# Kernel tuning notes

Measured on AMD Instinct MI355X. Metric: run time of the kernel, lower is better.

## Reference

```python
import jax, jax.numpy as jnp
import numpy as np

N = 50000  # num nodes
E = 800000  # num edges
D_IN = 128
D_OUT = 128
K = 2


def mean_propagate(x, src, dst):
    # scatter-mean over incoming edges: out[d] = mean_{(s,d) in edges} x[s]
    sums = jax.ops.segment_sum(x[src], dst, num_segments=N)  # [N, D]
    deg = jax.ops.segment_sum(jnp.ones((src.shape[0],), x.dtype), dst, num_segments=N)
    return sums / jnp.maximum(deg, 1.0)[:, None]


def setup_inputs() -> dict:
    key = jax.random.key(0)
    k1, k2, k3, k4 = jax.random.split(key, 4)
    x = jax.random.normal(k1, (N, D_IN), dtype=jnp.float32)
    edge_index = jax.random.randint(k2, (2, E), 0, N, dtype=jnp.int64)
    fan_in = D_IN * (K + 1)
    bound = 1.0 / np.sqrt(fan_in)
    W = jax.random.uniform(k3, (D_OUT, fan_in), dtype=jnp.float32, minval=-bound, maxval=bound)
    b = jax.random.uniform(k4, (D_OUT,), dtype=jnp.float32, minval=-bound, maxval=bound)
    return {"x": x, "edge_index": edge_index, "W": W, "b": b}


def reference(x, edge_index, W, b):
    src, dst = edge_index[0], edge_index[1]
    features = [x]
    propagated = x
    for _ in range(K):
        propagated = mean_propagate(propagated, src, dst)
        features.append(propagated)
    h = jnp.concatenate(features, axis=-1)  # [N, D_IN*(K+1)]
    return h @ W.T + b  # [N, D_OUT]
```

## Files before the change

### kernel.cpp

```cpp
#include <hip/hip_runtime.h>
#include <cstddef>


#define DFEAT 128
#define SUBSHIFT 8
#define MAXSUB 256
#define EPB 2048
#define CAP 16384

typedef __attribute__((ext_vector_type(8))) short short8v;
typedef __attribute__((ext_vector_type(4))) float f32x4;

__device__ inline unsigned short f2bf(float f) {
    unsigned int u;
    __builtin_memcpy(&u, &f, 4);
    unsigned int r = u + 0x7FFFu + ((u >> 16) & 1u);
    return (unsigned short)(r >> 16);
}
__device__ inline float bf2f(unsigned short h) {
    unsigned int u = ((unsigned int)h) << 16;
    float f;
    __builtin_memcpy(&f, &u, 4);
    return f;
}

__global__ void zero_kernel(int* __restrict__ p, int n) {
    int i = blockIdx.x * blockDim.x + threadIdx.x;
    if (i < n) p[i] = 0;
}

__global__ void conv_bf16_kernel(const float* __restrict__ in,
                                 unsigned short* __restrict__ outb, int total4) {
    int i = blockIdx.x * blockDim.x + threadIdx.x;
    if (i >= total4) return;
    const float4 v = reinterpret_cast<const float4*>(in)[i];
    unsigned int w0 = (unsigned int)f2bf(v.x) | ((unsigned int)f2bf(v.y) << 16);
    unsigned int w1 = (unsigned int)f2bf(v.z) | ((unsigned int)f2bf(v.w) << 16);
    reinterpret_cast<uint2*>(outb)[i] = make_uint2(w0, w1);
}

__global__ void pack_w_kernel(const float* __restrict__ W,
                              unsigned short* __restrict__ Wpk) {
    const int idx = blockIdx.x * blockDim.x + threadIdx.x;
    if (idx >= 6144) return;
    const int lane = idx & 63;
    const int nt = (idx >> 6) & 7;
    const int ks = idx >> 9;
    const int col = nt * 16 + (lane & 15);
    const int k = ks * 32 + (lane >> 4) * 8;
    const float* wp = W + (size_t)col * 384 + k;
    unsigned int w[4];
#pragma unroll
    for (int j = 0; j < 4; ++j) {
        w[j] = (unsigned int)f2bf(wp[2 * j]) |
               ((unsigned int)f2bf(wp[2 * j + 1]) << 16);
    }
    *reinterpret_cast<uint4*>(Wpk + (size_t)idx * 8) = make_uint4(w[0], w[1], w[2], w[3]);
}

__global__ __launch_bounds__(256) void partitionA_kernel(
    const int* __restrict__ src, const int* __restrict__ dst,
    int* __restrict__ subFill, int* __restrict__ subReal,
    uint2* __restrict__ staging, int E, int nsub) {
    __shared__ int cnt[MAXSUB];
    __shared__ int base[MAXSUB];
    const int t = threadIdx.x;
    for (int i = t; i < nsub; i += 256) cnt[i] = 0;
    __syncthreads();
    const int e0 = blockIdx.x * EPB;
    int d[8], s[8], b[8], rk[8];
#pragma unroll
    for (int j = 0; j < 8; ++j) {
        const int e = e0 + j * 256 + t;
        if (e < E) {
            d[j] = __builtin_nontemporal_load(dst + e);
            s[j] = __builtin_nontemporal_load(src + e);
            b[j] = d[j] >> SUBSHIFT;
            rk[j] = atomicAdd(&cnt[b[j]], 1);
        } else {
            d[j] = -1; s[j] = 0; b[j] = 0; rk[j] = 0;
        }
    }
    __syncthreads();
    for (int i = t; i < nsub; i += 256) {
        const int c = cnt[i];
        if (c > 0) {
            const int padded = (c + 15) & ~15;
            int bse = atomicAdd(&subFill[i], padded);
            if (bse + padded > CAP) bse = CAP - padded;
            base[i] = bse;
            atomicAdd(&subReal[i], c);
        }
    }
    __syncthreads();
#pragma unroll
    for (int j = 0; j < 8; ++j)
        if (d[j] >= 0)
            staging[(size_t)b[j] * CAP + base[b[j]] + rk[j]] =
                make_uint2((unsigned)d[j], (unsigned)s[j]);
    for (int i = t; i < nsub; i += 256) {
        const int c = cnt[i];
        if (c > 0) {
            const int padded = (c + 15) & ~15;
            for (int k = c; k < padded; ++k)
                staging[(size_t)i * CAP + base[i] + k] = make_uint2(0xFFFFFFFFu, 0u);
        }
    }
}

__global__ __launch_bounds__(256) void scanSub_kernel(const int* __restrict__ subReal,
                                                      int* __restrict__ subBase, int nsub) {
    __shared__ int s[256];
    const int t = threadIdx.x;
    const int v = (t < nsub) ? subReal[t] : 0;
    s[t] = v;
    __syncthreads();
#pragma unroll
    for (int off = 1; off < 256; off <<= 1) {
        int x = (t >= off) ? s[t - off] : 0;
        __syncthreads();
        s[t] += x;
        __syncthreads();
    }
    if (t < nsub) subBase[t] = s[t] - v;
}

__global__ __launch_bounds__(256) void partitionB_kernel(
    const uint2* __restrict__ staging, const int* __restrict__ subFill,
    const int* __restrict__ subBase, int* __restrict__ rowptr,
    float* __restrict__ inv, int* __restrict__ col, int N, int E) {
    __shared__ int cnt[1 << SUBSHIFT];
    __shared__ int loc[1 << SUBSHIFT];
    __shared__ int cur[1 << SUBSHIFT];
    const int b = blockIdx.x;
    const int n0 = b << SUBSHIFT;
    const int t = threadIdx.x;
    cnt[t] = 0;
    __syncthreads();
    const int fill = min(subFill[b], CAP);
    const uint2* seg = staging + (size_t)b * CAP;
    for (int i = t; i < fill; i += 256) {
        const unsigned dd = seg[i].x;
        if (dd != 0xFFFFFFFFu) atomicAdd(&cnt[dd - (unsigned)n0], 1);
    }
    __syncthreads();
    const int v = cnt[t];
    loc[t] = v;
    __syncthreads();
#pragma unroll
    for (int off = 1; off < 256; off <<= 1) {
        int x = (t >= off) ? loc[t - off] : 0;
        __syncthreads();
        loc[t] += x;
        __syncthreads();
    }
    const int gpos = subBase[b] + loc[t] - v;
    const int n = n0 + t;
    if (n < N) {
        rowptr[n] = gpos;
        inv[n] = 1.0f / (float)max(v, 1);
    }
    cur[t] = gpos;
    __syncthreads();
    for (int i = t; i < fill; i += 256) {
        const uint2 pr = seg[i];
        if (pr.x != 0xFFFFFFFFu) {
            const int pos = atomicAdd(&cur[(int)pr.x - n0], 1);
            col[pos] = (int)pr.y;
        }
    }
    if (b == 0 && t == 0) rowptr[N] = E;
}

__global__ __launch_bounds__(256) void gather_bf16_kernel(
    const unsigned short* __restrict__ feat, const int* __restrict__ rowptr,
    const int* __restrict__ col, const float* __restrict__ inv,
    unsigned short* __restrict__ outb, int N) {
    const int n = blockIdx.x * 16 + (threadIdx.x >> 4);
    const int lane = threadIdx.x & 15;
    if (n >= N) return;
    const int beg = rowptr[n];
    const int end = rowptr[n + 1];
    float acc[8];
#pragma unroll
    for (int j = 0; j < 8; ++j) acc[j] = 0.0f;
    int e = beg;
    for (; e + 1 < end; e += 2) {
        const int s0 = col[e];
        const int s1 = col[e + 1];
        const short8v v0 = *reinterpret_cast<const short8v*>(
            feat + (size_t)s0 * DFEAT + lane * 8);
        const short8v v1 = *reinterpret_cast<const short8v*>(
            feat + (size_t)s1 * DFEAT + lane * 8);
#pragma unroll
        for (int j = 0; j < 8; ++j)
            acc[j] += bf2f((unsigned short)v0[j]) + bf2f((unsigned short)v1[j]);
    }
    if (e < end) {
        const int s0 = col[e];
        const short8v v0 = *reinterpret_cast<const short8v*>(
            feat + (size_t)s0 * DFEAT + lane * 8);
#pragma unroll
        for (int j = 0; j < 8; ++j) acc[j] += bf2f((unsigned short)v0[j]);
    }
    const float sc = inv[n];
    unsigned int w[4];
#pragma unroll
    for (int j = 0; j < 4; ++j) {
        w[j] = (unsigned int)f2bf(acc[2 * j] * sc) |
               ((unsigned int)f2bf(acc[2 * j + 1] * sc) << 16);
    }
    *reinterpret_cast<uint4*>(outb + (size_t)n * DFEAT + lane * 8) =
        make_uint4(w[0], w[1], w[2], w[3]);
}

__global__ __launch_bounds__(256) void gemm_mfma_kernel(
    const unsigned short* __restrict__ xb, const unsigned short* __restrict__ m1b,
    const unsigned short* __restrict__ m2b, const unsigned short* __restrict__ Wpk,
    const float* __restrict__ bias, float* __restrict__ out, int N) {
    const int t = threadIdx.x;
    const int w = t >> 6;
    const int l = t & 63;
    const int lr = l & 15;
    const int kg = l >> 4;
    const int rowBase = blockIdx.x * 64 + w * 16;
    int arow = rowBase + lr;
    if (arow >= N) arow = N - 1;

    const short8v* Wv = reinterpret_cast<const short8v*>(Wpk);

    f32x4 acc[8];
#pragma unroll
    for (int nt = 0; nt < 8; ++nt) acc[nt] = (f32x4){0.f, 0.f, 0.f, 0.f};

#pragma unroll
    for (int ks = 0; ks < 12; ++ks) {
        const unsigned short* feat = (ks < 4) ? xb : (ks < 8 ? m1b : m2b);
        const int k0 = (ks & 3) * 32;
        const short8v a = *reinterpret_cast<const short8v*>(
            feat + (size_t)arow * DFEAT + k0 + kg * 8);
        short8v bfrag[8];
#pragma unroll
        for (int nt = 0; nt < 8; ++nt)
            bfrag[nt] = Wv[(ks * 8 + nt) * 64 + l];
#pragma unroll
        for (int nt = 0; nt < 8; ++nt)
            acc[nt] = __builtin_amdgcn_mfma_f32_16x16x32_bf16(a, bfrag[nt], acc[nt], 0, 0, 0);
    }

#pragma unroll
    for (int nt = 0; nt < 8; ++nt) {
        const int c = nt * 16 + lr;
        const float bv = bias[c];
#pragma unroll
        for (int r = 0; r < 4; ++r) {
            const int node = rowBase + kg * 4 + r;
            if (node < N) out[(size_t)node * DFEAT + c] = acc[nt][r] + bv;
        }
    }
}

extern "C" void kernel_launch(void* const* d_in, const int* in_sizes, int n_in,
                              void* d_out, int out_size, void* d_ws, size_t ws_size,
                              hipStream_t stream) {
    (void)n_in; (void)out_size; (void)ws_size;
    const float* x  = (const float*)d_in[0];
    const int*   ei = (const int*)d_in[1];
    const float* W  = (const float*)d_in[2];
    const float* b  = (const float*)d_in[3];
    float* out = (float*)d_out;

    const int N = in_sizes[0] / DFEAT;
    const int E = in_sizes[1] / 2;
    const int* src = ei;
    const int* dst = ei + E;
    const int nsub = (N + (1 << SUBSHIFT) - 1) >> SUBSHIFT;

    auto up = [](size_t v) { return (v + 255) & ~(size_t)255; };
    char* p = (char*)d_ws;
    int*   subFill   = (int*)p;            p += up((size_t)MAXSUB * 4 * 2);
    int*   subReal   = subFill + MAXSUB;
    int*   subBase   = (int*)p;            p += up((size_t)MAXSUB * 4);
    int*   rowptr    = (int*)p;            p += up(((size_t)N + 1) * 4);
    uint2* staging   = (uint2*)p;          p += up((size_t)MAXSUB * CAP * 8);
    int*   col       = (int*)p;            p += up((size_t)E * 4);
    float* inv       = (float*)p;          p += up((size_t)N * 4);
    unsigned short* xb  = (unsigned short*)p;  p += up((size_t)N * DFEAT * 2);
    unsigned short* m1b = (unsigned short*)p;  p += up((size_t)N * DFEAT * 2);
    unsigned short* m2b = (unsigned short*)p;  p += up((size_t)N * DFEAT * 2);
    unsigned short* Wpk = (unsigned short*)p;  p += up((size_t)6144 * 8 * 2);

    zero_kernel<<<1, 2 * MAXSUB, 0, stream>>>(subFill, 2 * MAXSUB);

    partitionA_kernel<<<(E + EPB - 1) / EPB, 256, 0, stream>>>(src, dst, subFill, subReal,
                                                               staging, E, nsub);
    scanSub_kernel<<<1, 256, 0, stream>>>(subReal, subBase, nsub);
    partitionB_kernel<<<nsub, 256, 0, stream>>>(staging, subFill, subBase,
                                                rowptr, inv, col, N, E);

    const int x4 = N * DFEAT / 4;
    conv_bf16_kernel<<<(x4 + 255) / 256, 256, 0, stream>>>(x, xb, x4);
    pack_w_kernel<<<(6144 + 255) / 256, 256, 0, stream>>>(W, Wpk);

    const int gatherBlocks = (N + 15) / 16;
    gather_bf16_kernel<<<gatherBlocks, 256, 0, stream>>>(xb,  rowptr, col, inv, m1b, N);
    gather_bf16_kernel<<<gatherBlocks, 256, 0, stream>>>(m1b, rowptr, col, inv, m2b, N);

    gemm_mfma_kernel<<<(N + 63) / 64, 256, 0, stream>>>(xb, m1b, m2b, Wpk, b, out, N);
}
```

Baseline: 142.0 us.

## Split bf16 features into 32-column planes and gather each plane separately

The bf16 feature matrices are stored as four planes of 32 columns, each 64 bytes per node, and each gather pass runs once per plane. A 50000-node plane is 3.2 MB, small enough to stay in cache, so the random per-edge reads should hit cache instead of going out to HBM. The cost is that the edge list is read four times per propagation and there are eight gather launches instead of two. Col loads and output stores are also switched to nontemporal hints, and the GEMM A-operand addressing is updated to match the plane layout.

```diff
diff --git a/kernel.cpp b/kernel.cpp
--- a/kernel.cpp
+++ b/kernel.cpp
@@ -10,6 +10,7 @@
 
 typedef __attribute__((ext_vector_type(8))) short short8v;
 typedef __attribute__((ext_vector_type(4))) float f32x4;
+typedef __attribute__((ext_vector_type(4))) unsigned int uint4v;
 
 __device__ inline unsigned short f2bf(float f) {
     unsigned int u;
@@ -29,14 +30,24 @@
     if (i < n) p[i] = 0;
 }
 
-__global__ void conv_bf16_kernel(const float* __restrict__ in,
-                                 unsigned short* __restrict__ outb, int total4) {
-    int i = blockIdx.x * blockDim.x + threadIdx.x;
-    if (i >= total4) return;
-    const float4 v = reinterpret_cast<const float4*>(in)[i];
-    unsigned int w0 = (unsigned int)f2bf(v.x) | ((unsigned int)f2bf(v.y) << 16);
-    unsigned int w1 = (unsigned int)f2bf(v.z) | ((unsigned int)f2bf(v.w) << 16);
-    reinterpret_cast<uint2*>(outb)[i] = make_uint2(w0, w1);
+__global__ void conv_q_kernel(const float* __restrict__ in,
+                              unsigned short* __restrict__ outb, int N) {
+    const int idx = blockIdx.x * blockDim.x + threadIdx.x;
+    const int perPlane = N * 4;
+    if (idx >= perPlane * 4) return;
+    const int q = idx / perPlane;
+    const int r = idx - q * perPlane;
+    const int n = r >> 2;
+    const int part = r & 3;
+    const float* s = in + (size_t)n * DFEAT + q * 32 + part * 8;
+    const float4 a = *reinterpret_cast<const float4*>(s);
+    const float4 b = *reinterpret_cast<const float4*>(s + 4);
+    uint4v w;
+    w.x = (unsigned)f2bf(a.x) | ((unsigned)f2bf(a.y) << 16);
+    w.y = (unsigned)f2bf(a.z) | ((unsigned)f2bf(a.w) << 16);
+    w.z = (unsigned)f2bf(b.x) | ((unsigned)f2bf(b.y) << 16);
+    w.w = (unsigned)f2bf(b.z) | ((unsigned)f2bf(b.w) << 16);
+    *reinterpret_cast<uint4v*>(outb + ((size_t)q * N + n) * 32 + part * 8) = w;
 }
 
 __global__ void pack_w_kernel(const float* __restrict__ W,
@@ -49,13 +60,12 @@
     const int col = nt * 16 + (lane & 15);
     const int k = ks * 32 + (lane >> 4) * 8;
     const float* wp = W + (size_t)col * 384 + k;
-    unsigned int w[4];
-#pragma unroll
-    for (int j = 0; j < 4; ++j) {
-        w[j] = (unsigned int)f2bf(wp[2 * j]) |
-               ((unsigned int)f2bf(wp[2 * j + 1]) << 16);
-    }
-    *reinterpret_cast<uint4*>(Wpk + (size_t)idx * 8) = make_uint4(w[0], w[1], w[2], w[3]);
+    uint4v w;
+    w.x = (unsigned)f2bf(wp[0]) | ((unsigned)f2bf(wp[1]) << 16);
+    w.y = (unsigned)f2bf(wp[2]) | ((unsigned)f2bf(wp[3]) << 16);
+    w.z = (unsigned)f2bf(wp[4]) | ((unsigned)f2bf(wp[5]) << 16);
+    w.w = (unsigned)f2bf(wp[6]) | ((unsigned)f2bf(wp[7]) << 16);
+    *reinterpret_cast<uint4v*>(Wpk + (size_t)idx * 8) = w;
 }
 
 __global__ __launch_bounds__(256) void partitionA_kernel(
@@ -172,12 +182,12 @@
     if (b == 0 && t == 0) rowptr[N] = E;
 }
 
-__global__ __launch_bounds__(256) void gather_bf16_kernel(
-    const unsigned short* __restrict__ feat, const int* __restrict__ rowptr,
+__global__ __launch_bounds__(256) void gather_q_kernel(
+    const unsigned short* __restrict__ featq, const int* __restrict__ rowptr,
     const int* __restrict__ col, const float* __restrict__ inv,
-    unsigned short* __restrict__ outb, int N) {
-    const int n = blockIdx.x * 16 + (threadIdx.x >> 4);
-    const int lane = threadIdx.x & 15;
+    unsigned short* __restrict__ outq, int N) {
+    const int n = blockIdx.x * 64 + (threadIdx.x >> 2);
+    const int lane = threadIdx.x & 3;
     if (n >= N) return;
     const int beg = rowptr[n];
     const int end = rowptr[n + 1];
@@ -186,32 +196,27 @@
     for (int j = 0; j < 8; ++j) acc[j] = 0.0f;
     int e = beg;
     for (; e + 1 < end; e += 2) {
-        const int s0 = col[e];
-        const int s1 = col[e + 1];
-        const short8v v0 = *reinterpret_cast<const short8v*>(
-            feat + (size_t)s0 * DFEAT + lane * 8);
-        const short8v v1 = *reinterpret_cast<const short8v*>(
-            feat + (size_t)s1 * DFEAT + lane * 8);
+        const int s0 = __builtin_nontemporal_load(col + e);
+        const int s1 = __builtin_nontemporal_load(col + e + 1);
+        const short8v v0 = *reinterpret_cast<const short8v*>(featq + (size_t)s0 * 32 + lane * 8);
+        const short8v v1 = *reinterpret_cast<const short8v*>(featq + (size_t)s1 * 32 + lane * 8);
 #pragma unroll
         for (int j = 0; j < 8; ++j)
             acc[j] += bf2f((unsigned short)v0[j]) + bf2f((unsigned short)v1[j]);
     }
     if (e < end) {
-        const int s0 = col[e];
-        const short8v v0 = *reinterpret_cast<const short8v*>(
-            feat + (size_t)s0 * DFEAT + lane * 8);
+        const int s0 = __builtin_nontemporal_load(col + e);
+        const short8v v0 = *reinterpret_cast<const short8v*>(featq + (size_t)s0 * 32 + lane * 8);
 #pragma unroll
         for (int j = 0; j < 8; ++j) acc[j] += bf2f((unsigned short)v0[j]);
     }
     const float sc = inv[n];
-    unsigned int w[4];
-#pragma unroll
-    for (int j = 0; j < 4; ++j) {
-        w[j] = (unsigned int)f2bf(acc[2 * j] * sc) |
-               ((unsigned int)f2bf(acc[2 * j + 1] * sc) << 16);
-    }
-    *reinterpret_cast<uint4*>(outb + (size_t)n * DFEAT + lane * 8) =
-        make_uint4(w[0], w[1], w[2], w[3]);
+    uint4v w;
+    w.x = (unsigned)f2bf(acc[0] * sc) | ((unsigned)f2bf(acc[1] * sc) << 16);
+    w.y = (unsigned)f2bf(acc[2] * sc) | ((unsigned)f2bf(acc[3] * sc) << 16);
+    w.z = (unsigned)f2bf(acc[4] * sc) | ((unsigned)f2bf(acc[5] * sc) << 16);
+    w.w = (unsigned)f2bf(acc[6] * sc) | ((unsigned)f2bf(acc[7] * sc) << 16);
+    __builtin_nontemporal_store(w, reinterpret_cast<uint4v*>(outq + (size_t)n * 32 + lane * 8));
 }
 
 __global__ __launch_bounds__(256) void gemm_mfma_kernel(
@@ -235,10 +240,10 @@
 
 #pragma unroll
     for (int ks = 0; ks < 12; ++ks) {
-        const unsigned short* feat = (ks < 4) ? xb : (ks < 8 ? m1b : m2b);
-        const int k0 = (ks & 3) * 32;
+        const unsigned short* fbase = (ks < 4) ? xb : (ks < 8 ? m1b : m2b);
+        const int q = ks & 3;
         const short8v a = *reinterpret_cast<const short8v*>(
-            feat + (size_t)arow * DFEAT + k0 + kg * 8);
+            fbase + ((size_t)q * N + arow) * 32 + kg * 8);
         short8v bfrag[8];
 #pragma unroll
         for (int nt = 0; nt < 8; ++nt)
@@ -298,13 +303,18 @@
     partitionB_kernel<<<nsub, 256, 0, stream>>>(staging, subFill, subBase,
                                                 rowptr, inv, col, N, E);
 
-    const int x4 = N * DFEAT / 4;
-    conv_bf16_kernel<<<(x4 + 255) / 256, 256, 0, stream>>>(x, xb, x4);
+    const int cq = N * 16;
+    conv_q_kernel<<<(cq + 255) / 256, 256, 0, stream>>>(x, xb, N);
     pack_w_kernel<<<(6144 + 255) / 256, 256, 0, stream>>>(W, Wpk);
 
-    const int gatherBlocks = (N + 15) / 16;
-    gather_bf16_kernel<<<gatherBlocks, 256, 0, stream>>>(xb,  rowptr, col, inv, m1b, N);
-    gather_bf16_kernel<<<gatherBlocks, 256, 0, stream>>>(m1b, rowptr, col, inv, m2b, N);
+    const int gBlocks = (N + 63) / 64;
+    const size_t plane = (size_t)N * 32;
+    for (int q = 0; q < 4; ++q)
+        gather_q_kernel<<<gBlocks, 256, 0, stream>>>(xb + q * plane, rowptr, col, inv,
+                                                     m1b + q * plane, N);
+    for (int q = 0; q < 4; ++q)
+        gather_q_kernel<<<gBlocks, 256, 0, stream>>>(m1b + q * plane, rowptr, col, inv,
+                                                     m2b + q * plane, N);
 
     gemm_mfma_kernel<<<(N + 63) / 64, 256, 0, stream>>>(xb, m1b, m2b, Wpk, b, out, N);
 }
```

Result: slower. 216.5 us (+52.5%).
